# Optimization experiments

Measured on AMD Instinct MI355X. Metric: run time of the kernel, lower is better.

## Reference

```python
import jax, jax.numpy as jnp
import numpy as np

B, N, D, E, G, MID, OUT = 8, 256, 128, 128, 128, 128, 128


def setup_inputs() -> dict:
    key = jax.random.key(0)
    ks = jax.random.split(key, 20)
    s = 0.02
    inp = {
        'node_fts': jax.random.normal(ks[0], (B, N, D), jnp.float32),
        'edge_fts': jax.random.normal(ks[1], (B, N, N, E), jnp.float32),
        'graph_fts': jax.random.normal(ks[2], (B, G), jnp.float32),
        'adj_mat': jax.random.randint(ks[3], (B, N, N), 0, 2, jnp.int32),
        'hidden': jax.random.normal(ks[4], (B, N, D), jnp.float32),
        # message linears (m_n_1, m_h_1, m_e_1, m_g_1)
        'Wn': s * jax.random.normal(ks[5], (D, MID), jnp.float32),
        'bn': jnp.zeros((MID,), jnp.float32),
        'Wh': s * jax.random.normal(ks[6], (D, MID), jnp.float32),
        'bh': jnp.zeros((MID,), jnp.float32),
        'We': s * jax.random.normal(ks[7], (E, MID), jnp.float32),
        'be': jnp.zeros((MID,), jnp.float32),
        'Wg': s * jax.random.normal(ks[8], (G, MID), jnp.float32),
        'bg': jnp.zeros((MID,), jnp.float32),
        # output linears o1 (node), o2 (hidden), o3 (msgs)
        'Wo1': s * jax.random.normal(ks[9], (D, OUT), jnp.float32),
        'bo1': jnp.zeros((OUT,), jnp.float32),
        'Wo2': s * jax.random.normal(ks[10], (D, OUT), jnp.float32),
        'bo2': jnp.zeros((OUT,), jnp.float32),
        'Wo3': s * jax.random.normal(ks[11], (MID, OUT), jnp.float32),
        'bo3': jnp.zeros((OUT,), jnp.float32),
    }
    return inp


def reference(node_fts, edge_fts, graph_fts, adj_mat, hidden,
              Wn, bn, Wh, bh, We, be, Wg, bg,
              Wo1, bo1, Wo2, bo2, Wo3, bo3):
    # Linear projections feeding the broadcast message tensor
    msg_n = node_fts @ Wn + bn          # (B, N, MID)
    msg_h = hidden @ Wh + bh            # (B, N, MID)
    msg_e = edge_fts @ We + be          # (B, N, N, MID)
    msg_g = graph_fts @ Wg + bg         # (B, MID)

    # Broadcast-add into (B, N, N, MID): axis1 <- msg_n (sender), axis2 <- msg_h
    msgs = (msg_n[:, None, :, :] + msg_h[:, :, None, :]
            + msg_e + msg_g[:, None, None, :])

    # Masked max-reduce over axis 1 (msgs_mlp_sizes is None -> no MLP)
    adj = adj_mat.astype(msgs.dtype)[..., None]  # (B, N, N, 1)
    msgs = jnp.max(msgs * adj, axis=1)           # (B, N, MID)

    ret = (node_fts @ Wo1 + bo1) + (hidden @ Wo2 + bo2) + (msgs @ Wo3 + bo3)
    return ret
```

## Files before the change

kernel.cpp:

```cpp
#include <hip/hip_runtime.h>
#include <hip/hip_bf16.h>

#define B_ 8
#define N_ 256
#define C_ 128
#define S_ 8
#define STEPB (N_ * C_ * 4)

typedef __attribute__((ext_vector_type(4))) float f32x4;
typedef __attribute__((ext_vector_type(2))) float f32x2;
typedef __attribute__((ext_vector_type(8))) short s16x8;

typedef __attribute__((address_space(1))) const void gas_void;
typedef __attribute__((address_space(3))) void las_void;

__device__ __forceinline__ unsigned short f2bf(float f) {
  unsigned int u = __builtin_bit_cast(unsigned int, f);
  u += 0x7FFFu + ((u >> 16) & 1u);
  return (unsigned short)(u >> 16);
}

__device__ __forceinline__ unsigned int pk2(float a, float b) {
  __hip_bfloat162 h = __float22bfloat162_rn(make_float2(a, b));
  unsigned int u;
  __builtin_memcpy(&u, &h, 4);
  return u;
}

__device__ __forceinline__ s16x8 cvt8(f32x4 lo, f32x4 hi) {
  union { unsigned int u[4]; s16x8 s; } r;
  r.u[0] = pk2(lo[0], lo[1]);
  r.u[1] = pk2(lo[2], lo[3]);
  r.u[2] = pk2(hi[0], hi[1]);
  r.u[3] = pk2(hi[2], hi[3]);
  return r.s;
}

__global__ void k_pro(const float* __restrict__ node, const float* __restrict__ hidden,
                      const float* __restrict__ graph,
                      const float* __restrict__ Wn, const float* __restrict__ bn,
                      const float* __restrict__ Wh, const float* __restrict__ bh,
                      const float* __restrict__ be,
                      const float* __restrict__ Wg, const float* __restrict__ bg,
                      const float* __restrict__ We,
                      float* __restrict__ ws_c, float* __restrict__ ws_mh2,
                      short* __restrict__ ws_B) {
  int bid = blockIdx.x, t = threadIdx.x;
  if (bid >= 512) {
    int f = bid - 512;
    if (t < 64) {
      int kb = f >> 3, nbg = f & 7;
      int lr = t & 15, lg = t >> 4;
      s16x8 v;
#pragma unroll
      for (int e = 0; e < 8; ++e)
        v[e] = (short)f2bf(We[(kb * 32 + lg * 8 + e) * C_ + nbg * 16 + lr]);
      *reinterpret_cast<s16x8*>(ws_B + (f * 64 + t) * 8) = v;
    }
    return;
  }
  bool isc = bid < 256;
  int row0 = (isc ? bid : bid - 256) * 8;
  const float* src = isc ? node : hidden;
  const float* W   = isc ? Wn : Wh;
  __shared__ float sh[8][C_];
#pragma unroll
  for (int r = 0; r < 8; ++r) sh[r][t] = src[(row0 + r) * C_ + t];
  __syncthreads();
  float g = 0.f;
  float acc[8];
#pragma unroll
  for (int r = 0; r < 8; ++r) acc[r] = 0.f;
  const float* gr = graph + (row0 >> 8) * C_;
  for (int k = 0; k < C_; k += 8) {
    float wv[8];
#pragma unroll
    for (int u = 0; u < 8; ++u) wv[u] = W[(k + u) * C_ + t];
    if (isc) {
      float wgv[8];
#pragma unroll
      for (int u = 0; u < 8; ++u) wgv[u] = Wg[(k + u) * C_ + t];
#pragma unroll
      for (int u = 0; u < 8; ++u) g += gr[k + u] * wgv[u];
    }
#pragma unroll
    for (int u = 0; u < 8; ++u)
#pragma unroll
      for (int r = 0; r < 8; ++r) acc[r] += sh[r][k + u] * wv[u];
  }
  if (isc) {
    float init = bn[t] + be[t] + bg[t] + g;
#pragma unroll
    for (int r = 0; r < 8; ++r) ws_c[(row0 + r) * C_ + t] = acc[r] + init;
  } else {
    float init = bh[t];
    int p = (t >> 5) * 32 + (t & 15) * 2 + ((t >> 4) & 1);
#pragma unroll
    for (int r = 0; r < 8; ++r) ws_mh2[(row0 + r) * C_ + p] = acc[r] + init;
  }
}

__global__ __launch_bounds__(256, 4) void k_main(
    const float* __restrict__ edge, const int* __restrict__ adjm,
    const short* __restrict__ ws_B,
    const float* __restrict__ ws_c, const float* __restrict__ ws_mh2,
    float* __restrict__ pbuf) {
  __shared__ __align__(16) char smem[3 * 8192];
  const int lane = threadIdx.x & 63;
  const int w = threadIdx.x >> 6;
  const int wg = blockIdx.x;
  const int s   = wg & 7;
  const int j16 = (wg >> 3) & 15;
  const int b   = wg >> 7;
  const int j0 = j16 * 16;
  const int n0 = w * 32;
  const int i0 = s * 32;
  const int lr = lane & 15;
  const int lg = lane >> 4;

  s16x8 bfrag[4][2];
#pragma unroll
  for (int kb = 0; kb < 4; ++kb)
#pragma unroll
    for (int nb = 0; nb < 2; ++nb)
      bfrag[kb][nb] = *reinterpret_cast<const s16x8*>(
          ws_B + ((kb * 8 + w * 2 + nb) * 64 + lane) * 8);

  float cf[2][4];
#pragma unroll
  for (int nb = 0; nb < 2; ++nb)
#pragma unroll
    for (int r = 0; r < 4; ++r)
      cf[nb][r] = ws_c[(b * N_ + j0 + lg * 4 + r) * C_ + n0 + nb * 16 + lr];

  f32x4 mx[2];
#pragma unroll
  for (int nb = 0; nb < 2; ++nb)
#pragma unroll
    for (int r = 0; r < 4; ++r) mx[nb][r] = -INFINITY;

  const char* gedge = (const char*)(edge + ((size_t)(b * N_ + i0) * N_ + j0) * C_);
  const float* mh2 = ws_mh2 + ((size_t)(b * N_) + i0) * C_ + n0 + lr * 2;
  const int* adjb = adjm + ((size_t)(b * N_) + i0) * N_ + j0 + lg * 4;

  int soff[2];
#pragma unroll
  for (int q = 0; q < 2; ++q) {
    int y = w * 2048 + q * 1024 + lane * 16;
    int row = y >> 9;
    soff[q] = y ^ ((row & 7) << 4);
  }
  const int base0 = lr * 512 + lg * 32;
  const int swz = (lr & 7) << 4;

  f32x2 mreg[3];
  int4  areg[3];

#define GLL16(GP, LP) __builtin_amdgcn_global_load_lds((gas_void*)(GP), (las_void*)(LP), 16, 0, 0)

#define ISSUE(SL, TT) do { \
    const char* gch = gedge + (size_t)(TT) * STEPB; \
    char* lb = smem + (SL) * 8192 + w * 2048; \
    GLL16(gch + soff[0], lb); \
    GLL16(gch + soff[1], lb + 1024); \
    mreg[SL] = *reinterpret_cast<const f32x2*>(mh2 + (size_t)(TT) * C_); \
    areg[SL] = *reinterpret_cast<const int4*>(adjb + (size_t)(TT) * N_); \
  } while (0)

#define STEP(SL, ISL, WAITN, DOISSUE, TI) do { \
    asm volatile("s_waitcnt vmcnt(" WAITN ")\n\ts_barrier" ::: "memory"); \
    if (DOISSUE) ISSUE(ISL, TI); \
    const char* rb = smem + (SL) * 8192; \
    s16x8 af[4]; \
    _Pragma("unroll") \
    for (int kb = 0; kb < 4; ++kb) { \
      int a0 = (base0 + kb * 128) ^ swz; \
      f32x4 lo = *reinterpret_cast<const f32x4*>(rb + a0); \
      f32x4 hi = *reinterpret_cast<const f32x4*>(rb + (a0 ^ 16)); \
      af[kb] = cvt8(lo, hi); \
    } \
    f32x2 mh = mreg[SL]; \
    int4 av = areg[SL]; \
    float adjf[4] = {(float)av.x, (float)av.y, (float)av.z, (float)av.w}; \
    _Pragma("unroll") \
    for (int nb = 0; nb < 2; ++nb) { \
      f32x4 acc; \
      _Pragma("unroll") \
      for (int r = 0; r < 4; ++r) acc[r] = cf[nb][r] + mh[nb]; \
      _Pragma("unroll") \
      for (int kb = 0; kb < 4; ++kb) \
        acc = __builtin_amdgcn_mfma_f32_16x16x32_bf16(af[kb], bfrag[kb][nb], acc, 0, 0, 0); \
      _Pragma("unroll") \
      for (int r = 0; r < 4; ++r) mx[nb][r] = fmaxf(mx[nb][r], adjf[r] * acc[r]); \
    } \
  } while (0)

  ISSUE(0, 0);
  ISSUE(1, 1);

  for (int o = 0; o < 10; ++o) {
    STEP(0, 2, "4", 1, 3 * o + 2);
    STEP(1, 0, "4", 1, 3 * o + 3);
    STEP(2, 1, "4", 1, 3 * o + 4);
  }
  STEP(0, 2, "4", 0, 0);
  STEP(1, 0, "0", 0, 0);

#undef STEP
#undef ISSUE
#undef GLL16

  float* prow = pbuf + (((size_t)s * B_ + b) * N_ + j0 + lg * 4) * C_ + n0 + lr;
#pragma unroll
  for (int nb = 0; nb < 2; ++nb)
#pragma unroll
    for (int r = 0; r < 4; ++r)
      prow[r * C_ + nb * 16] = mx[nb][r];
}

__global__ void k_epi(const float* __restrict__ node, const float* __restrict__ hidden,
                      const float* __restrict__ Wo1, const float* __restrict__ bo1,
                      const float* __restrict__ Wo2, const float* __restrict__ bo2,
                      const float* __restrict__ Wo3, const float* __restrict__ bo3,
                      const float* __restrict__ pbuf, float* __restrict__ out) {
  int row0 = blockIdx.x * 4;
  int col = threadIdx.x & 127;
  int half = threadIdx.x >> 7;
  __shared__ float shn[4][C_], shh[4][C_], shm[4][C_];
#pragma unroll
  for (int r = 0; r < 2; ++r) {
    int rr = half * 2 + r;
    shn[rr][col] = node[(row0 + rr) * C_ + col];
    shh[rr][col] = hidden[(row0 + rr) * C_ + col];
    float mv = -INFINITY;
#pragma unroll
    for (int s = 0; s < S_; ++s)
      mv = fmaxf(mv, pbuf[((size_t)s * (B_ * N_) + row0 + rr) * C_ + col]);
    shm[rr][col] = mv;
  }
  __syncthreads();
  float init = bo1[col] + bo2[col] + bo3[col];
  float acc[2];
  acc[0] = init; acc[1] = init;
  for (int k = 0; k < C_; k += 8) {
    float wv1[8], wv2[8], wv3[8];
#pragma unroll
    for (int u = 0; u < 8; ++u) {
      wv1[u] = Wo1[(k + u) * C_ + col];
      wv2[u] = Wo2[(k + u) * C_ + col];
      wv3[u] = Wo3[(k + u) * C_ + col];
    }
#pragma unroll
    for (int u = 0; u < 8; ++u)
#pragma unroll
      for (int r = 0; r < 2; ++r) {
        int rr = half * 2 + r;
        acc[r] += shn[rr][k + u] * wv1[u] + shh[rr][k + u] * wv2[u] + shm[rr][k + u] * wv3[u];
      }
  }
#pragma unroll
  for (int r = 0; r < 2; ++r)
    out[(row0 + half * 2 + r) * C_ + col] = acc[r];
}

extern "C" void kernel_launch(void* const* d_in, const int* in_sizes, int n_in,
                              void* d_out, int out_size, void* d_ws, size_t ws_size,
                              hipStream_t stream) {
  const float* node   = (const float*)d_in[0];
  const float* edge   = (const float*)d_in[1];
  const float* graph  = (const float*)d_in[2];
  const int*   adjm   = (const int*)d_in[3];
  const float* hidden = (const float*)d_in[4];
  const float* Wn = (const float*)d_in[5];  const float* bn = (const float*)d_in[6];
  const float* Wh = (const float*)d_in[7];  const float* bh = (const float*)d_in[8];
  const float* We = (const float*)d_in[9];  const float* be = (const float*)d_in[10];
  const float* Wg = (const float*)d_in[11]; const float* bg = (const float*)d_in[12];
  const float* Wo1 = (const float*)d_in[13]; const float* bo1 = (const float*)d_in[14];
  const float* Wo2 = (const float*)d_in[15]; const float* bo2 = (const float*)d_in[16];
  const float* Wo3 = (const float*)d_in[17]; const float* bo3 = (const float*)d_in[18];
  float* out = (float*)d_out;

  char* ws = (char*)d_ws;
  float* ws_c   = (float*)ws;
  float* ws_mh2 = (float*)(ws + (1u << 20));
  short* ws_B   = (short*)(ws + (2u << 20));
  float* pbuf   = (float*)(ws + (4u << 20));

  k_pro<<<544, 128, 0, stream>>>(node, hidden, graph, Wn, bn, Wh, bh, be, Wg, bg, We,
                                 ws_c, ws_mh2, ws_B);
  k_main<<<1024, 256, 0, stream>>>(edge, adjm, ws_B, ws_c, ws_mh2, pbuf);
  k_epi<<<512, 256, 0, stream>>>(node, hidden, Wo1, bo1, Wo2, bo2, Wo3, bo3,
                                 pbuf, out);
}
```

Baseline: 87.81 us.

## Preload bf16 hidden-messages and byte-packed adjacency into LDS once per block

The prologue kernel now stores the hidden-message projection as bf16 and packs the int32 adjacency matrix into bytes in extra blocks. The main kernel loads both slices into LDS once at the start with global_load_lds, instead of issuing per-step register loads alongside the edge tile pipeline. This removes two global loads per pipeline step and lowers the vmcnt wait depth. In exchange it adds a conversion pass over the adjacency, uses more LDS per block (which may reduce occupancy), and rounds the hidden-message term to bf16, losing some precision.

```diff
diff --git a/kernel.cpp b/kernel.cpp
--- a/kernel.cpp
+++ b/kernel.cpp
@@ -8,7 +8,6 @@
 #define STEPB (N_ * C_ * 4)
 
 typedef __attribute__((ext_vector_type(4))) float f32x4;
-typedef __attribute__((ext_vector_type(2))) float f32x2;
 typedef __attribute__((ext_vector_type(8))) short s16x8;
 
 typedef __attribute__((address_space(1))) const void gas_void;
@@ -37,15 +36,25 @@
 }
 
 __global__ void k_pro(const float* __restrict__ node, const float* __restrict__ hidden,
-                      const float* __restrict__ graph,
+                      const float* __restrict__ graph, const int* __restrict__ adjm,
                       const float* __restrict__ Wn, const float* __restrict__ bn,
                       const float* __restrict__ Wh, const float* __restrict__ bh,
                       const float* __restrict__ be,
                       const float* __restrict__ Wg, const float* __restrict__ bg,
                       const float* __restrict__ We,
-                      float* __restrict__ ws_c, float* __restrict__ ws_mh2,
-                      short* __restrict__ ws_B) {
+                      float* __restrict__ ws_c, unsigned short* __restrict__ ws_mh2,
+                      short* __restrict__ ws_B, unsigned char* __restrict__ ws_adj) {
   int bid = blockIdx.x, t = threadIdx.x;
+  if (bid >= 544) {
+    int base = (bid - 544) * 1024 + t * 8;
+    int4 a = *reinterpret_cast<const int4*>(adjm + base);
+    int4 c = *reinterpret_cast<const int4*>(adjm + base + 4);
+    uint2 v;
+    v.x = (unsigned)a.x | ((unsigned)a.y << 8) | ((unsigned)a.z << 16) | ((unsigned)a.w << 24);
+    v.y = (unsigned)c.x | ((unsigned)c.y << 8) | ((unsigned)c.z << 16) | ((unsigned)c.w << 24);
+    *reinterpret_cast<uint2*>(ws_adj + base) = v;
+    return;
+  }
   if (bid >= 512) {
     int f = bid - 512;
     if (t < 64) {
@@ -96,16 +105,19 @@
     float init = bh[t];
     int p = (t >> 5) * 32 + (t & 15) * 2 + ((t >> 4) & 1);
 #pragma unroll
-    for (int r = 0; r < 8; ++r) ws_mh2[(row0 + r) * C_ + p] = acc[r] + init;
+    for (int r = 0; r < 8; ++r) ws_mh2[(row0 + r) * C_ + p] = f2bf(acc[r] + init);
   }
 }
 
 __global__ __launch_bounds__(256, 4) void k_main(
-    const float* __restrict__ edge, const int* __restrict__ adjm,
+    const float* __restrict__ edge, const unsigned char* __restrict__ ws_adj,
     const short* __restrict__ ws_B,
-    const float* __restrict__ ws_c, const float* __restrict__ ws_mh2,
+    const float* __restrict__ ws_c, const unsigned short* __restrict__ ws_mh2,
     float* __restrict__ pbuf) {
-  __shared__ __align__(16) char smem[3 * 8192];
+  __shared__ __align__(16) char smem[3 * 8192 + 8192 + 512];
+  char* ring    = smem;
+  char* mh_lds  = smem + 24576;
+  char* adj_lds = smem + 24576 + 8192;
   const int lane = threadIdx.x & 63;
   const int w = threadIdx.x >> 6;
   const int wg = blockIdx.x;
@@ -140,8 +152,6 @@
     for (int r = 0; r < 4; ++r) mx[nb][r] = -INFINITY;
 
   const char* gedge = (const char*)(edge + ((size_t)(b * N_ + i0) * N_ + j0) * C_);
-  const float* mh2 = ws_mh2 + ((size_t)(b * N_) + i0) * C_ + n0 + lr * 2;
-  const int* adjb = adjm + ((size_t)(b * N_) + i0) * N_ + j0 + lg * 4;
 
   int soff[2];
 #pragma unroll
@@ -153,24 +163,32 @@
   const int base0 = lr * 512 + lg * 32;
   const int swz = (lr & 7) << 4;
 
-  f32x2 mreg[3];
-  int4  areg[3];
-
 #define GLL16(GP, LP) __builtin_amdgcn_global_load_lds((gas_void*)(GP), (las_void*)(LP), 16, 0, 0)
+#define GLL4(GP, LP)  __builtin_amdgcn_global_load_lds((gas_void*)(GP), (las_void*)(LP), 4, 0, 0)
 
 #define ISSUE(SL, TT) do { \
     const char* gch = gedge + (size_t)(TT) * STEPB; \
-    char* lb = smem + (SL) * 8192 + w * 2048; \
+    char* lb = ring + (SL) * 8192 + w * 2048; \
     GLL16(gch + soff[0], lb); \
     GLL16(gch + soff[1], lb + 1024); \
-    mreg[SL] = *reinterpret_cast<const f32x2*>(mh2 + (size_t)(TT) * C_); \
-    areg[SL] = *reinterpret_cast<const int4*>(adjb + (size_t)(TT) * N_); \
   } while (0)
 
-#define STEP(SL, ISL, WAITN, DOISSUE, TI) do { \
+  {
+    const char* mh_g = (const char*)(ws_mh2 + ((size_t)(b * N_) + i0) * C_);
+    GLL16(mh_g + w * 2048 + lane * 16, mh_lds + w * 2048);
+    GLL16(mh_g + w * 2048 + 1024 + lane * 16, mh_lds + w * 2048 + 1024);
+    const char* adj_g = (const char*)(ws_adj + ((size_t)(b * N_) + i0) * N_ + j0);
+    GLL4(adj_g + (lane >> 2) * N_ + (lane & 3) * 4, adj_lds);
+    GLL4(adj_g + ((lane >> 2) + 16) * N_ + (lane & 3) * 4, adj_lds + 256);
+  }
+  ISSUE(0, 0);
+  ISSUE(1, 1);
+  asm volatile("s_waitcnt vmcnt(4)\n\ts_barrier" ::: "memory");
+
+#define STEP(SL, ISL, WAITN, DOISSUE, TI, T) do { \
     asm volatile("s_waitcnt vmcnt(" WAITN ")\n\ts_barrier" ::: "memory"); \
     if (DOISSUE) ISSUE(ISL, TI); \
-    const char* rb = smem + (SL) * 8192; \
+    const char* rb = ring + (SL) * 8192; \
     s16x8 af[4]; \
     _Pragma("unroll") \
     for (int kb = 0; kb < 4; ++kb) { \
@@ -179,14 +197,18 @@
       f32x4 hi = *reinterpret_cast<const f32x4*>(rb + (a0 ^ 16)); \
       af[kb] = cvt8(lo, hi); \
     } \
-    f32x2 mh = mreg[SL]; \
-    int4 av = areg[SL]; \
-    float adjf[4] = {(float)av.x, (float)av.y, (float)av.z, (float)av.w}; \
+    unsigned int mw = *reinterpret_cast<const unsigned int*>(mh_lds + (T) * 256 + w * 64 + lr * 4); \
+    unsigned int ab = *reinterpret_cast<const unsigned int*>(adj_lds + (T) * 16 + lg * 4); \
+    float mh0 = __builtin_bit_cast(float, mw << 16); \
+    float mh1 = __builtin_bit_cast(float, mw & 0xffff0000u); \
+    float adjf[4] = {(float)(ab & 0xff), (float)((ab >> 8) & 0xff), \
+                     (float)((ab >> 16) & 0xff), (float)(ab >> 24)}; \
     _Pragma("unroll") \
     for (int nb = 0; nb < 2; ++nb) { \
       f32x4 acc; \
+      float mhv = nb ? mh1 : mh0; \
       _Pragma("unroll") \
-      for (int r = 0; r < 4; ++r) acc[r] = cf[nb][r] + mh[nb]; \
+      for (int r = 0; r < 4; ++r) acc[r] = cf[nb][r] + mhv; \
       _Pragma("unroll") \
       for (int kb = 0; kb < 4; ++kb) \
         acc = __builtin_amdgcn_mfma_f32_16x16x32_bf16(af[kb], bfrag[kb][nb], acc, 0, 0, 0); \
@@ -195,20 +217,18 @@
     } \
   } while (0)
 
-  ISSUE(0, 0);
-  ISSUE(1, 1);
-
   for (int o = 0; o < 10; ++o) {
-    STEP(0, 2, "4", 1, 3 * o + 2);
-    STEP(1, 0, "4", 1, 3 * o + 3);
-    STEP(2, 1, "4", 1, 3 * o + 4);
-  }
-  STEP(0, 2, "4", 0, 0);
-  STEP(1, 0, "0", 0, 0);
+    STEP(0, 2, "2", 1, 3 * o + 2, 3 * o);
+    STEP(1, 0, "2", 1, 3 * o + 3, 3 * o + 1);
+    STEP(2, 1, "2", 1, 3 * o + 4, 3 * o + 2);
+  }
+  STEP(0, 2, "2", 0, 0, 30);
+  STEP(1, 0, "0", 0, 0, 31);
 
 #undef STEP
 #undef ISSUE
 #undef GLL16
+#undef GLL4
 
   float* prow = pbuf + (((size_t)s * B_ + b) * N_ + j0 + lg * 4) * C_ + n0 + lr;
 #pragma unroll
@@ -281,14 +301,15 @@
   float* out = (float*)d_out;
 
   char* ws = (char*)d_ws;
-  float* ws_c   = (float*)ws;
-  float* ws_mh2 = (float*)(ws + (1u << 20));
-  short* ws_B   = (short*)(ws + (2u << 20));
-  float* pbuf   = (float*)(ws + (4u << 20));
-
-  k_pro<<<544, 128, 0, stream>>>(node, hidden, graph, Wn, bn, Wh, bh, be, Wg, bg, We,
-                                 ws_c, ws_mh2, ws_B);
-  k_main<<<1024, 256, 0, stream>>>(edge, adjm, ws_B, ws_c, ws_mh2, pbuf);
+  float*          ws_c   = (float*)ws;
+  unsigned short* ws_mh2 = (unsigned short*)(ws + (1u << 20));
+  short*          ws_B   = (short*)(ws + 1572864u);
+  unsigned char*  ws_adj = (unsigned char*)(ws + 1835008u);
+  float*          pbuf   = (float*)(ws + (4u << 20));
+
+  k_pro<<<1056, 128, 0, stream>>>(node, hidden, graph, adjm, Wn, bn, Wh, bh, be,
+                                  Wg, bg, We, ws_c, ws_mh2, ws_B, ws_adj);
+  k_main<<<1024, 256, 0, stream>>>(edge, ws_adj, ws_B, ws_c, ws_mh2, pbuf);
   k_epi<<<512, 256, 0, stream>>>(node, hidden, Wo1, bo1, Wo2, bo2, Wo3, bo3,
                                  pbuf, out);
 }
```

Result: no change. 88.14 us (+0.4%).
